# Performance work log

Measured on AMD Instinct MI355X. Metric: run time of the kernel, lower is better.

Reference implementation:

```python
import jax, jax.numpy as jnp
import numpy as np

V, DW, DH, OUT = 50000, 300, 50, 4
B, T = 1024, 200


def setup_inputs() -> dict:
    key = jax.random.key(0)
    ks = jax.random.split(key, 9)
    x = jax.random.randint(ks[0], (B, T), 0, V)
    lengs = jax.random.randint(ks[1], (B,), 1, T + 1)  # valid lengths >= 1
    k = 1.0 / np.sqrt(DH)
    emb = jax.random.normal(ks[2], (V, DW), jnp.float32)
    emb = emb.at[0].set(0.0)  # padding_idx=0
    w_ih = jax.random.uniform(ks[3], (4 * DH, DW), jnp.float32, -k, k)
    w_hh = jax.random.uniform(ks[4], (4 * DH, DH), jnp.float32, -k, k)
    b_ih = jax.random.uniform(ks[5], (4 * DH,), jnp.float32, -k, k)
    b_hh = jax.random.uniform(ks[6], (4 * DH,), jnp.float32, -k, k)
    w_out = jax.random.uniform(ks[7], (OUT, DH), jnp.float32, -k, k)
    b_out = jax.random.uniform(ks[8], (OUT,), jnp.float32, -k, k)
    return {"x": x, "lengs": lengs, "emb": emb, "w_ih": w_ih, "w_hh": w_hh,
            "b_ih": b_ih, "b_hh": b_hh, "w_out": w_out, "b_out": b_out}


def reference(x, lengs, emb, w_ih, w_hh, b_ih, b_hh, w_out, b_out):
    b, t = x.shape
    xe = emb[x]                                        # [B,T,DW]
    mask = jnp.arange(t)[None, :] < lengs[:, None]     # [B,T] valid steps
    bias = b_ih + b_hh                                 # [4*DH]

    def step(carry, inp):
        h, c = carry
        x_t, m_t = inp                                 # [B,DW], [B]
        g = x_t @ w_ih.T + h @ w_hh.T + bias           # [B,4*DH]
        i, f, gg, o = jnp.split(g, 4, axis=-1)         # torch gate order i,f,g,o
        c_new = jax.nn.sigmoid(f) * c + jax.nn.sigmoid(i) * jnp.tanh(gg)
        h_new = jax.nn.sigmoid(o) * jnp.tanh(c_new)
        m = m_t[:, None]
        # packed-sequence semantics: state frozen past each sequence's length
        return (jnp.where(m, h_new, h), jnp.where(m, c_new, c)), None

    h0 = jnp.zeros((b, DH), xe.dtype)
    (h, _), _ = jax.lax.scan(step, (h0, h0),
                             (xe.transpose(1, 0, 2), mask.T))
    logits = h @ w_out.T + b_out                       # hidden.view(B,-1) -> Linear
    return jax.nn.softmax(logits, axis=1)
```

## Files before the change

kernel.cpp:

```cpp
#include <hip/hip_runtime.h>
#include <math.h>

#define VOCAB 50000
#define DW 300
#define DH 50
#define G4 200
#define BATCH 1024
#define TMAX 200
#define OUTC 4

__global__ __launch_bounds__(256) void transpose_wih(
    const float* __restrict__ w_ih, float* __restrict__ w_T)
{
    int i = blockIdx.x * 256 + threadIdx.x;
    if (i < G4 * DW) {
        int u = i / DW, k = i % DW;
        w_T[k * G4 + u] = w_ih[i];
    }
}

__global__ __launch_bounds__(256, 2) void proj_kernel(
    const float* __restrict__ emb, const float* __restrict__ w_T,
    const float* __restrict__ b_ih, const float* __restrict__ b_hh,
    float* __restrict__ emb_proj)
{
    __shared__ __align__(16) float e_s[100 * 108];
    const int tid = threadIdx.x;
    const int v0 = blockIdx.x * 100;
    const int m_idx = tid / 25;
    const int n_idx = tid % 25;

    float acc[10][8];
#pragma unroll
    for (int m = 0; m < 10; m++)
#pragma unroll
        for (int c = 0; c < 8; c++) acc[m][c] = 0.f;

    for (int kc = 0; kc < DW; kc += 100) {
        __syncthreads();
        for (int i = tid; i < 2500; i += 256) {
            int r = i / 25, c = i % 25;
            float4 v = *(const float4*)&emb[(size_t)(v0 + r) * DW + kc + c * 4];
            *(float4*)&e_s[r * 108 + c * 4] = v;
        }
        __syncthreads();

        if (tid < 250) {
#pragma unroll 2
            for (int kk = 0; kk < 25; kk++) {
                float4 e4[10];
#pragma unroll
                for (int m = 0; m < 10; m++)
                    e4[m] = *(const float4*)&e_s[(m_idx * 10 + m) * 108 + kk * 4];
                const float* wbase = w_T + (size_t)(kc + kk * 4) * G4 + n_idx * 8;
#pragma unroll
                for (int j = 0; j < 4; j++) {
                    float4 wa = *(const float4*)(wbase + j * G4);
                    float4 wb = *(const float4*)(wbase + j * G4 + 4);
#pragma unroll
                    for (int m = 0; m < 10; m++) {
                        float ev = (j == 0) ? e4[m].x : (j == 1) ? e4[m].y
                                 : (j == 2) ? e4[m].z : e4[m].w;
                        acc[m][0] = fmaf(ev, wa.x, acc[m][0]);
                        acc[m][1] = fmaf(ev, wa.y, acc[m][1]);
                        acc[m][2] = fmaf(ev, wa.z, acc[m][2]);
                        acc[m][3] = fmaf(ev, wa.w, acc[m][3]);
                        acc[m][4] = fmaf(ev, wb.x, acc[m][4]);
                        acc[m][5] = fmaf(ev, wb.y, acc[m][5]);
                        acc[m][6] = fmaf(ev, wb.z, acc[m][6]);
                        acc[m][7] = fmaf(ev, wb.w, acc[m][7]);
                    }
                }
            }
        }
    }

    if (tid < 250) {
#pragma unroll
        for (int c = 0; c < 8; c++) {
            int u = n_idx * 8 + c;
            float bias = b_ih[u] + b_hh[u];
            int u2 = (u % DH) * 4 + (u / DH);
#pragma unroll
            for (int m = 0; m < 10; m++)
                emb_proj[(size_t)(v0 + m_idx * 10 + m) * G4 + u2] = acc[m][c] + bias;
        }
    }
}

__device__ __forceinline__ float dpp_xor1(float x) {
    return __int_as_float(__builtin_amdgcn_update_dpp(
        0, __float_as_int(x), 0xB1, 0xF, 0xF, true));
}

__global__ __launch_bounds__(128, 2) void lstm_kernel(
    const int* __restrict__ x, const int* __restrict__ lengs,
    const float* __restrict__ emb_proj, const float* __restrict__ w_hh,
    const float* __restrict__ w_out, const float* __restrict__ b_out,
    float* __restrict__ out)
{
    __shared__ __align__(16) float hbuf[2][52];
    __shared__ int x_s[TMAX];
    __shared__ float red[OUTC];

    const int tid = threadIdx.x;
    const int b   = blockIdx.x;
    const int u   = tid >> 1;
    const int uu  = (u < DH) ? u : 0;
    const int odd = tid & 1;
    const int len = lengs[b];

    for (int i = tid; i < TMAX; i += 128) x_s[i] = x[b * TMAX + i];
    if (tid < 52) hbuf[0][tid] = 0.f;

    float wA[DH], wB[DH];
    {
        const float* rA = w_hh + (size_t)((2 * odd) * DH + uu) * DH;
        const float* rB = w_hh + (size_t)((2 * odd + 1) * DH + uu) * DH;
#pragma unroll
        for (int k = 0; k < 25; k++) {
            float2 a  = *(const float2*)(rA + 2 * k);
            float2 bb = *(const float2*)(rB + 2 * k);
            wA[2 * k] = a.x;  wA[2 * k + 1] = a.y;
            wB[2 * k] = bb.x; wB[2 * k + 1] = bb.y;
        }
    }
    __syncthreads();

    const int col = (u < DH) ? (tid * 2) : 0;
    const float* ep = emb_proj;
    float2 p0 = *(const float2*)(ep + (size_t)x_s[0] * G4 + col);
    float2 p1 = *(const float2*)(ep + (size_t)x_s[1] * G4 + col);
    float2 p2 = *(const float2*)(ep + (size_t)x_s[2] * G4 + col);
    float c_reg = 0.f;

    for (int t = 0; t < len; t++) {
        float2 cur = p0; p0 = p1; p1 = p2;
        int nt = t + 3; nt = (nt < TMAX) ? nt : TMAX - 1;
        p2 = *(const float2*)(ep + (size_t)x_s[nt] * G4 + col);

        const float* hb = hbuf[t & 1];
        float accA0 = 0.f, accA1 = 0.f, accB0 = 0.f, accB1 = 0.f;
#pragma unroll
        for (int k4 = 0; k4 < 12; k4++) {
            float4 h4 = *(const float4*)(hb + 4 * k4);
            if ((k4 & 1) == 0) {
                accA0 = fmaf(h4.x, wA[4*k4], fmaf(h4.y, wA[4*k4+1],
                        fmaf(h4.z, wA[4*k4+2], fmaf(h4.w, wA[4*k4+3], accA0))));
                accB0 = fmaf(h4.x, wB[4*k4], fmaf(h4.y, wB[4*k4+1],
                        fmaf(h4.z, wB[4*k4+2], fmaf(h4.w, wB[4*k4+3], accB0))));
            } else {
                accA1 = fmaf(h4.x, wA[4*k4], fmaf(h4.y, wA[4*k4+1],
                        fmaf(h4.z, wA[4*k4+2], fmaf(h4.w, wA[4*k4+3], accA1))));
                accB1 = fmaf(h4.x, wB[4*k4], fmaf(h4.y, wB[4*k4+1],
                        fmaf(h4.z, wB[4*k4+2], fmaf(h4.w, wB[4*k4+3], accB1))));
            }
        }
        {
            float2 h2 = *(const float2*)(hb + 48);
            accA0 = fmaf(h2.x, wA[48], fmaf(h2.y, wA[49], accA0));
            accB1 = fmaf(h2.x, wB[48], fmaf(h2.y, wB[49], accB1));
        }
        float gA = cur.x + accA0 + accA1;
        float gB = cur.y + accB0 + accB1;

        float yA = odd ? 2.f * gA : gA;
        float sA = 1.f / (1.f + __expf(-yA));
        float vA = odd ? fmaf(2.f, sA, -1.f) : sA;
        float vB = 1.f / (1.f + __expf(-gB));

        float oA = dpp_xor1(vA);
        float oB = dpp_xor1(vB);
        float si = odd ? oA : vA;
        float sf = odd ? oB : vB;
        float tg = odd ? vA : oA;
        float so = odd ? vB : oB;

        float cn = fmaf(sf, c_reg, si * tg);
        c_reg = cn;
        float th = fmaf(2.f, 1.f / (1.f + __expf(-2.f * cn)), -1.f);
        float hn = so * th;
        if (!odd && u < DH) hbuf[(t + 1) & 1][u] = hn;
        __syncthreads();
    }

    const float* hf = hbuf[len & 1];
    if (tid < OUTC) {
        float lg = b_out[tid];
        const float* wo = w_out + tid * DH;
#pragma unroll
        for (int k = 0; k < DH; k++) lg = fmaf(hf[k], wo[k], lg);
        red[tid] = lg;
    }
    if (tid < OUTC) {
        float m = fmaxf(fmaxf(red[0], red[1]), fmaxf(red[2], red[3]));
        float s = 0.f;
#pragma unroll
        for (int j = 0; j < OUTC; j++) s += __expf(red[j] - m);
        out[b * OUTC + tid] = __expf(red[tid] - m) / s;
    }
}

extern "C" void kernel_launch(void* const* d_in, const int* in_sizes, int n_in,
                              void* d_out, int out_size, void* d_ws, size_t ws_size,
                              hipStream_t stream) {
    const int*   x     = (const int*)d_in[0];
    const int*   lengs = (const int*)d_in[1];
    const float* emb   = (const float*)d_in[2];
    const float* w_ih  = (const float*)d_in[3];
    const float* w_hh  = (const float*)d_in[4];
    const float* b_ih  = (const float*)d_in[5];
    const float* b_hh  = (const float*)d_in[6];
    const float* w_out = (const float*)d_in[7];
    const float* b_out = (const float*)d_in[8];
    float* out = (float*)d_out;

    float* emb_proj = (float*)d_ws;
    float* w_T      = emb_proj + (size_t)VOCAB * G4;

    hipLaunchKernelGGL(transpose_wih, dim3((G4 * DW + 255) / 256), dim3(256),
                       0, stream, w_ih, w_T);
    hipLaunchKernelGGL(proj_kernel, dim3(VOCAB / 100), dim3(256), 0, stream,
                       emb, w_T, b_ih, b_hh, emb_proj);
    hipLaunchKernelGGL(lstm_kernel, dim3(BATCH), dim3(128), 0, stream,
                       x, lengs, emb_proj, w_hh, w_out, b_out, out);
}
```

Baseline: 330.9 us.

## Permute w_ih columns at transpose, prefetch weights, vectorize projection stores

The gate-interleaving permutation moves into the w_ih transpose, so the projection kernel can write emb_proj rows as contiguous float4 stores instead of scattered scalar stores. The projection inner loop now double-buffers the weight loads from global memory, prefetching the next k-slice's weights while computing the current one. In the LSTM kernel, empty asm constraints pin the recurrent weights in VGPRs so the compiler does not rematerialize or spill them. The prefetch raises register pressure in the projection kernel, which may lower occupancy.

```diff
diff --git a/kernel.cpp b/kernel.cpp
--- a/kernel.cpp
+++ b/kernel.cpp
@@ -15,7 +15,8 @@
     int i = blockIdx.x * 256 + threadIdx.x;
     if (i < G4 * DW) {
         int u = i / DW, k = i % DW;
-        w_T[k * G4 + u] = w_ih[i];
+        int u2 = (u % DH) * 4 + (u / DH);
+        w_T[k * G4 + u2] = w_ih[i];
     }
 }
 
@@ -36,6 +37,8 @@
 #pragma unroll
         for (int c = 0; c < 8; c++) acc[m][c] = 0.f;
 
+    const float* wcol = w_T + n_idx * 8;
+
     for (int kc = 0; kc < DW; kc += 100) {
         __syncthreads();
         for (int i = tid; i < 2500; i += 256) {
@@ -46,44 +49,63 @@
         __syncthreads();
 
         if (tid < 250) {
-#pragma unroll 2
+            float4 wa[4], wb[4];
+#pragma unroll
+            for (int j = 0; j < 4; j++) {
+                const float* p = wcol + (size_t)(kc + j) * G4;
+                wa[j] = *(const float4*)p;
+                wb[j] = *(const float4*)(p + 4);
+            }
             for (int kk = 0; kk < 25; kk++) {
+                float4 na[4], nb[4];
+                int kn = kc + ((kk < 24) ? (kk + 1) : kk) * 4;
+#pragma unroll
+                for (int j = 0; j < 4; j++) {
+                    const float* p = wcol + (size_t)(kn + j) * G4;
+                    na[j] = *(const float4*)p;
+                    nb[j] = *(const float4*)(p + 4);
+                }
                 float4 e4[10];
 #pragma unroll
                 for (int m = 0; m < 10; m++)
                     e4[m] = *(const float4*)&e_s[(m_idx * 10 + m) * 108 + kk * 4];
-                const float* wbase = w_T + (size_t)(kc + kk * 4) * G4 + n_idx * 8;
 #pragma unroll
                 for (int j = 0; j < 4; j++) {
-                    float4 wa = *(const float4*)(wbase + j * G4);
-                    float4 wb = *(const float4*)(wbase + j * G4 + 4);
 #pragma unroll
                     for (int m = 0; m < 10; m++) {
                         float ev = (j == 0) ? e4[m].x : (j == 1) ? e4[m].y
                                  : (j == 2) ? e4[m].z : e4[m].w;
-                        acc[m][0] = fmaf(ev, wa.x, acc[m][0]);
-                        acc[m][1] = fmaf(ev, wa.y, acc[m][1]);
-                        acc[m][2] = fmaf(ev, wa.z, acc[m][2]);
-                        acc[m][3] = fmaf(ev, wa.w, acc[m][3]);
-                        acc[m][4] = fmaf(ev, wb.x, acc[m][4]);
-                        acc[m][5] = fmaf(ev, wb.y, acc[m][5]);
-                        acc[m][6] = fmaf(ev, wb.z, acc[m][6]);
-                        acc[m][7] = fmaf(ev, wb.w, acc[m][7]);
+                        acc[m][0] = fmaf(ev, wa[j].x, acc[m][0]);
+                        acc[m][1] = fmaf(ev, wa[j].y, acc[m][1]);
+                        acc[m][2] = fmaf(ev, wa[j].z, acc[m][2]);
+                        acc[m][3] = fmaf(ev, wa[j].w, acc[m][3]);
+                        acc[m][4] = fmaf(ev, wb[j].x, acc[m][4]);
+                        acc[m][5] = fmaf(ev, wb[j].y, acc[m][5]);
+                        acc[m][6] = fmaf(ev, wb[j].z, acc[m][6]);
+                        acc[m][7] = fmaf(ev, wb[j].w, acc[m][7]);
                     }
                 }
+#pragma unroll
+                for (int j = 0; j < 4; j++) { wa[j] = na[j]; wb[j] = nb[j]; }
             }
         }
     }
 
     if (tid < 250) {
+        float bias[8];
 #pragma unroll
         for (int c = 0; c < 8; c++) {
-            int u = n_idx * 8 + c;
-            float bias = b_ih[u] + b_hh[u];
-            int u2 = (u % DH) * 4 + (u / DH);
-#pragma unroll
-            for (int m = 0; m < 10; m++)
-                emb_proj[(size_t)(v0 + m_idx * 10 + m) * G4 + u2] = acc[m][c] + bias;
+            int u2 = n_idx * 8 + c;
+            int u  = (u2 & 3) * DH + (u2 >> 2);
+            bias[c] = b_ih[u] + b_hh[u];
+        }
+#pragma unroll
+        for (int m = 0; m < 10; m++) {
+            float* dst = &emb_proj[(size_t)(v0 + m_idx * 10 + m) * G4 + n_idx * 8];
+            *(float4*)dst = make_float4(acc[m][0] + bias[0], acc[m][1] + bias[1],
+                                        acc[m][2] + bias[2], acc[m][3] + bias[3]);
+            *(float4*)(dst + 4) = make_float4(acc[m][4] + bias[4], acc[m][5] + bias[5],
+                                              acc[m][6] + bias[6], acc[m][7] + bias[7]);
         }
     }
 }
@@ -124,6 +146,11 @@
             wA[2 * k] = a.x;  wA[2 * k + 1] = a.y;
             wB[2 * k] = bb.x; wB[2 * k + 1] = bb.y;
         }
+    }
+#pragma unroll
+    for (int k = 0; k < DH; k++) {
+        asm volatile("" : "+v"(wA[k]));
+        asm volatile("" : "+v"(wB[k]));
     }
     __syncthreads();
 
```

After: 307.1 us. 7.2% less time.
